# Performance work log

Measured on AMD Instinct MI355X. Metric: run time of the kernel, lower is better.

## Reference

```python
import jax, jax.numpy as jnp
import numpy as np

IN_CHANNELS = 3
WINDOW_SIZE = 11
SIGMA = 1.5
PAD = WINDOW_SIZE // 2


def _create_window():
    # NOTE: faithful to the original repo, the exponent is POSITIVE (a known
    # bug in AntixK/PyTorch-VAE); we replicate the exact math.
    x = np.arange(WINDOW_SIZE, dtype=np.float64)
    k = np.exp((x - WINDOW_SIZE // 2) ** 2 / (2.0 * SIGMA ** 2))
    k = (k / k.sum()).astype(np.float32)
    w2d = np.outer(k, k)  # [K, K]
    # depthwise kernel, OIHW with groups=C -> [C, 1, K, K]
    return jnp.asarray(np.broadcast_to(w2d, (IN_CHANNELS, 1, WINDOW_SIZE, WINDOW_SIZE)).copy())


def _dwconv(x, w):
    return jax.lax.conv_general_dilated(
        x, w, window_strides=(1, 1), padding=[(PAD, PAD), (PAD, PAD)],
        feature_group_count=IN_CHANNELS,
        dimension_numbers=('NCHW', 'OIHW', 'NCHW'))


def _avg_pool2(x):
    B, C, H, W = x.shape
    return x.reshape(B, C, H // 2, 2, W // 2, 2).mean(axis=(3, 5))


def _ssim(img1, img2, window):
    mu1 = _dwconv(img1, window)
    mu2 = _dwconv(img2, window)
    mu1_sq = mu1 * mu1
    mu2_sq = mu2 * mu2
    mu1_mu2 = mu1 * mu2
    sigma1_sq = _dwconv(img1 * img1, window) - mu1_sq
    sigma2_sq = _dwconv(img2 * img2, window) - mu2_sq
    sigma12 = _dwconv(img1 * img2, window) - mu1_mu2
    C1 = 0.01 ** 2
    C2 = 0.03 ** 2
    v1 = 2.0 * sigma12 + C2
    v2 = sigma1_sq + sigma2_sq + C2
    cs = jnp.mean(v1 / v2)
    ssim_map = (2.0 * mu1_mu2 + C1) * v1 / ((mu1_sq + mu2_sq + C1) * v2)
    return jnp.mean(ssim_map), cs  # size_average=True


def setup_inputs() -> dict:
    key = jax.random.key(0)
    k1, k2 = jax.random.split(key)
    shape = (32, 3, 512, 512)
    img1 = jax.random.uniform(k1, shape, dtype=jnp.float32)
    img2 = jax.random.uniform(k2, shape, dtype=jnp.float32)
    return {"img1": img1, "img2": img2}


def reference(img1, img2):
    weights = jnp.asarray([0.0448, 0.2856, 0.3001, 0.2363, 0.1333], dtype=jnp.float32)
    window = _create_window()
    mssim, mcs = [], []
    for _ in range(5):
        sim, cs = _ssim(img1, img2, window)
        mssim.append(sim)
        mcs.append(cs)
        img1 = _avg_pool2(img1)
        img2 = _avg_pool2(img2)
    mssim = jnp.stack(mssim)
    mcs = jnp.stack(mcs)
    pow1 = mcs ** weights
    pow2 = mssim ** weights
    output = jnp.prod(pow1[:-1] * pow2[-1])
    return 1.0 - output
```

## Files before the change

kernel.cpp:

```cpp
#include <hip/hip_runtime.h>
#include <cmath>

typedef short bf16x8 __attribute__((ext_vector_type(8)));
typedef float f32x4 __attribute__((ext_vector_type(4)));

struct Coeffs { float k[11]; };

__device__ __forceinline__ ushort f2bf(float f) {
    unsigned u = __float_as_uint(f);
    u += 0x7fff + ((u >> 16) & 1);
    return (ushort)(u >> 16);
}

__device__ __forceinline__ unsigned pk2(float lo, float hi) {
    unsigned d;
    asm("v_cvt_pk_bf16_f32 %0, %1, %2" : "=v"(d) : "v"(lo), "v"(hi));
    return d;
}

__device__ __forceinline__ float frcp(float x) { return __builtin_amdgcn_rcpf(x); }

__device__ __forceinline__ float4 ld4s(const float* __restrict__ p, int r, int c, int H, int W) {
    float4 v = make_float4(0.f, 0.f, 0.f, 0.f);
    if (r >= 0 && r < H) {
        const float* row = p + (size_t)r * W;
        if (c >= 0 && c + 3 < W) {
            v = *reinterpret_cast<const float4*>(row + c);
        } else {
            if (c + 0 >= 0 && c + 0 < W) v.x = row[c + 0];
            if (c + 1 >= 0 && c + 1 < W) v.y = row[c + 1];
            if (c + 2 >= 0 && c + 2 < W) v.z = row[c + 2];
            if (c + 3 >= 0 && c + 3 < W) v.w = row[c + 3];
        }
    }
    return v;
}

union FragU { ushort us[8]; bf16x8 v; uint4 q; };
union RdU   { uint4 q; bf16x8 v; };

__global__ __launch_bounds__(64)
void init_frag_kernel(uint4* __restrict__ tab, Coeffs cf) {
    const int lane = threadIdx.x;
    const int lj   = lane & 15;
    const int part = lane >> 4;
    FragU bHf, aVf;
    #pragma unroll
    for (int i = 0; i < 8; ++i) {
        const int kk = part * 8 + i;
        const int tH = kk - lj - 3;
        const int tV = kk - lj;
        float vH = 0.f, vV = 0.f;
        #pragma unroll
        for (int tt = 0; tt < 11; ++tt) {
            vH = (tH == tt) ? cf.k[tt] : vH;
            vV = (tV == tt) ? cf.k[tt] : vV;
        }
        bHf.us[i] = f2bf(vH);
        aVf.us[i] = f2bf(vV);
    }
    tab[lane]      = bHf.q;
    tab[64 + lane] = aVf.q;
}

__device__ __forceinline__ void stage_load(const float* __restrict__ p1,
                                           const float* __restrict__ p2,
                                           int H, int W, int gr, int gc0,
                                           float (&a)[12], float (&b)[12]) {
    if (gr >= 0 && gr < H && gc0 >= 0 && gc0 + 12 <= W) {
        const size_t idx = (size_t)gr * W + gc0;
        #pragma unroll
        for (int g = 0; g < 3; ++g) {
            float4 va = *reinterpret_cast<const float4*>(p1 + idx + 4 * g);
            float4 vb = *reinterpret_cast<const float4*>(p2 + idx + 4 * g);
            a[4*g+0]=va.x; a[4*g+1]=va.y; a[4*g+2]=va.z; a[4*g+3]=va.w;
            b[4*g+0]=vb.x; b[4*g+1]=vb.y; b[4*g+2]=vb.z; b[4*g+3]=vb.w;
        }
    } else {
        #pragma unroll
        for (int g = 0; g < 3; ++g) {
            float4 va = ld4s(p1, gr, gc0 + 4 * g, H, W);
            float4 vb = ld4s(p2, gr, gc0 + 4 * g, H, W);
            a[4*g+0]=va.x; a[4*g+1]=va.y; a[4*g+2]=va.z; a[4*g+3]=va.w;
            b[4*g+0]=vb.x; b[4*g+1]=vb.y; b[4*g+2]=vb.z; b[4*g+3]=vb.w;
        }
    }
}

__device__ __forceinline__ void stage_write(const float (&a)[12], const float (&b)[12],
                                            char* q0, char* q1, char* q2) {
    unsigned pks[2][6];
    #pragma unroll
    for (int e = 0; e < 6; ++e) {
        pks[0][e] = pk2(a[2*e], a[2*e+1]);
        pks[1][e] = pk2(b[2*e], b[2*e+1]);
    }
    #pragma unroll
    for (int s = 0; s < 2; ++s) {
        *(uint2*)(q0 + s * 6144) = make_uint2(pks[s][0], pks[s][1]);
        *(uint2*)(q1 + s * 6144) = make_uint2(pks[s][2], pks[s][3]);
        *(uint2*)(q2 + s * 6144) = make_uint2(pks[s][4], pks[s][5]);
    }
}

__device__ __forceinline__ void h_phase(const char* a0p, const char* a1p, char* st,
                                        const bf16x8 bH, const f32x4 zf) {
    #pragma unroll
    for (int cg = 0; cg < 2; ++cg) {
        const char* ap = cg ? a1p : a0p;
        uint4 da = *(const uint4*)(ap);
        uint4 db = *(const uint4*)(ap + 6144);
        unsigned wa[4] = {da.x, da.y, da.z, da.w};
        unsigned wb[4] = {db.x, db.y, db.z, db.w};
        uint4 qaa, qbb, qab;
        unsigned* paa = &qaa.x; unsigned* pbb = &qbb.x; unsigned* pab = &qab.x;
        #pragma unroll
        for (int e = 0; e < 4; ++e) {
            const float alo = __uint_as_float(wa[e] << 16);
            const float ahi = __uint_as_float(wa[e] & 0xffff0000u);
            const float blo = __uint_as_float(wb[e] << 16);
            const float bhi = __uint_as_float(wb[e] & 0xffff0000u);
            paa[e] = pk2(alo * alo, ahi * ahi);
            pbb[e] = pk2(blo * blo, bhi * bhi);
            pab[e] = pk2(alo * blo, ahi * bhi);
        }
        RdU f0, f1, f2, f3, f4;
        f0.q = da; f1.q = db; f2.q = qaa; f3.q = qbb; f4.q = qab;
        f32x4 d0 = __builtin_amdgcn_mfma_f32_16x16x32_bf16(f0.v, bH, zf, 0, 0, 0);
        f32x4 d1 = __builtin_amdgcn_mfma_f32_16x16x32_bf16(f1.v, bH, zf, 0, 0, 0);
        f32x4 d2 = __builtin_amdgcn_mfma_f32_16x16x32_bf16(f2.v, bH, zf, 0, 0, 0);
        f32x4 d3 = __builtin_amdgcn_mfma_f32_16x16x32_bf16(f3.v, bH, zf, 0, 0, 0);
        f32x4 d4 = __builtin_amdgcn_mfma_f32_16x16x32_bf16(f4.v, bH, zf, 0, 0, 0);
        char* sc = st + cg * 2048;
        *(uint2*)(sc)          = make_uint2(pk2(d0[0], d0[1]), pk2(d0[2], d0[3]));
        *(uint2*)(sc + 4096)   = make_uint2(pk2(d1[0], d1[1]), pk2(d1[2], d1[3]));
        *(uint2*)(sc + 8192)   = make_uint2(pk2(d2[0], d2[1]), pk2(d2[2], d2[3]));
        *(uint2*)(sc + 12288)  = make_uint2(pk2(d3[0], d3[1]), pk2(d3[2], d3[3]));
        *(uint2*)(sc + 16384)  = make_uint2(pk2(d4[0], d4[1]), pk2(d4[2], d4[3]));
    }
}

__device__ __forceinline__ void v_phase(const char* hb, const bf16x8 aV, const f32x4 zf,
                                        float& ssim_acc, float& cs_acc) {
    f32x4 acc[5];
    #pragma unroll
    for (int s = 0; s < 5; ++s) {
        RdU br;
        br.q = *(const uint4*)(hb + s * 4096);
        acc[s] = __builtin_amdgcn_mfma_f32_16x16x32_bf16(aV, br.v, zf, 0, 0, 0);
    }
    const float C1 = 1e-4f, C2 = 9e-4f;
    #pragma unroll
    for (int r = 0; r < 4; ++r) {
        const float mu1 = acc[0][r], mu2 = acc[1][r];
        const float m11 = acc[2][r], m22 = acc[3][r], m12 = acc[4][r];
        const float mu1s = mu1 * mu1, mu2s = mu2 * mu2, mu12 = mu1 * mu2;
        const float v1 = 2.f * (m12 - mu12) + C2;
        const float v2 = (m11 - mu1s) + (m22 - mu2s) + C2;
        const float r2 = frcp(v2);
        const float rd = frcp(mu1s + mu2s + C1);
        cs_acc   += v1 * r2;
        ssim_acc += (2.f * mu12 + C1) * v1 * r2 * rd;
    }
}

__device__ __forceinline__ void pool_load8(const float* __restrict__ p1,
                                           const float* __restrict__ p2,
                                           size_t idx, int W, float4 (&P)[8]) {
    P[0] = *reinterpret_cast<const float4*>(p1 + idx);
    P[1] = *reinterpret_cast<const float4*>(p1 + idx + 4);
    P[2] = *reinterpret_cast<const float4*>(p1 + idx + W);
    P[3] = *reinterpret_cast<const float4*>(p1 + idx + W + 4);
    P[4] = *reinterpret_cast<const float4*>(p2 + idx);
    P[5] = *reinterpret_cast<const float4*>(p2 + idx + 4);
    P[6] = *reinterpret_cast<const float4*>(p2 + idx + W);
    P[7] = *reinterpret_cast<const float4*>(p2 + idx + W + 4);
}

__device__ __forceinline__ void pool_store8(const float4 (&P)[8],
                                            float* __restrict__ o1, float* __restrict__ o2,
                                            int bc, int H, int W, int r0, int c0t,
                                            int i, int h) {
    float4 oa, ob;
    oa.x = 0.25f*(P[0].x+P[0].y+P[2].x+P[2].y); oa.y = 0.25f*(P[0].z+P[0].w+P[2].z+P[2].w);
    oa.z = 0.25f*(P[1].x+P[1].y+P[3].x+P[3].y); oa.w = 0.25f*(P[1].z+P[1].w+P[3].z+P[3].w);
    ob.x = 0.25f*(P[4].x+P[4].y+P[6].x+P[6].y); ob.y = 0.25f*(P[4].z+P[4].w+P[6].z+P[6].w);
    ob.z = 0.25f*(P[5].x+P[5].y+P[7].x+P[7].y); ob.w = 0.25f*(P[5].z+P[5].w+P[7].z+P[7].w);
    const int W2 = W >> 1;
    const size_t base = (size_t)bc * (size_t)(H >> 1) * W2
                      + (size_t)(r0/2 + i) * W2 + (c0t/2 + 4*h);
    *reinterpret_cast<float4*>(o1 + base) = oa;
    *reinterpret_cast<float4*>(o2 + base) = ob;
}

__global__ __launch_bounds__(256)
void ssim_level0_mfma(const float* __restrict__ i1, const float* __restrict__ i2,
                      float* __restrict__ o1, float* __restrict__ o2,
                      int H, int W,
                      double* __restrict__ accum,
                      const uint4* __restrict__ frag_tab)
{
    __shared__ __align__(16) ushort A_lds[2][48][64];
    __shared__ __align__(16) ushort H_T [5][32][64];
    __shared__ double red[2][4];

    const int tid  = threadIdx.x;
    const int lane = tid & 63;
    const int lj   = lane & 15;
    const int part = lane >> 4;
    const int swz  = (lane & 7) << 4;
    const int wv   = __builtin_amdgcn_readfirstlane(tid) >> 6;

    const int bc = blockIdx.z;
    const int r0 = blockIdx.y * 32;
    const int c0 = blockIdx.x * 64;
    const float* p1 = i1 + (size_t)bc * H * W;
    const float* p2 = i2 + (size_t)bc * H * W;

    RdU bHu, aVu;
    bHu.q = frag_tab[lane];
    aVu.q = frag_tab[64 + lane];
    const bf16x8 bH = bHu.v;
    const bf16x8 aV = aVu.v;
    const f32x4 zf = {0.f, 0.f, 0.f, 0.f};

    float ssim_acc = 0.f, cs_acc = 0.f;

    float aB[12], bB[12];
    char *q0 = nullptr, *q1 = nullptr, *q2 = nullptr;
    if (tid < 192) {
        const int row_rel = tid >> 2;
        const int colg    = tid & 3;
        const int gr  = r0 - 5 + row_rel;
        const int gcA = c0 - 8 + 12 * colg;
        float aA[12], bA[12];
        stage_load(p1, p2, H, W, gr, gcA,      aA, bA);
        stage_load(p1, p2, H, W, gr, gcA + 32, aB, bB);
        const int cb   = 24 * colg;
        const int swzr = (row_rel & 7) << 4;
        char* base0 = (char*)&A_lds[0][0][0] + row_rel * 128;
        q0 = base0 + ((cb)      ^ swzr);
        q1 = base0 + ((cb + 8)  ^ swzr);
        q2 = base0 + ((cb + 16) ^ swzr);
        stage_write(aA, bA, q0, q1, q2);
    } else if (o1 != nullptr) {
        const int p = tid - 192;
        const int i = p & 15;
        const int h = p >> 4;
        const size_t idxA = (size_t)(r0 + 2 * i) * W + (c0 + 8 * h);
        float4 PA[8], PB[8];
        pool_load8(p1, p2, idxA,      W, PA);
        pool_load8(p1, p2, idxA + 32, W, PB);
        pool_store8(PA, o1, o2, bc, H, W, r0, c0,      i, h);
        pool_store8(PB, o1, o2, bc, H, W, r0, c0 + 32, i, h);
    }
    __syncthreads();

    const char* Ab  = (const char*)&A_lds[0][0][0] + wv * 2048 + lj * 128;
    const char* a0p = Ab + ((part * 16)      ^ swz);
    const char* a1p = Ab + ((32 + part * 16) ^ swz);
    char* st = (char*)&H_T[0][0][0] + lj * 128 + ((wv * 32 + part * 8) ^ swz);
    const int rg2 = wv >> 1, cg2 = wv & 1;
    const char* hb = (const char*)&H_T[0][0][0] + cg2 * 2048 + lj * 128
                   + ((rg2 * 32 + part * 16) ^ swz);

    if (wv < 3) h_phase(a0p, a1p, st, bH, zf);
    __syncthreads();

    if (tid < 192) stage_write(aB, bB, q0, q1, q2);
    v_phase(hb, aV, zf, ssim_acc, cs_acc);
    __syncthreads();

    if (wv < 3) h_phase(a0p, a1p, st, bH, zf);
    __syncthreads();

    v_phase(hb, aV, zf, ssim_acc, cs_acc);

    #pragma unroll
    for (int off = 32; off > 0; off >>= 1) {
        ssim_acc += __shfl_down(ssim_acc, off);
        cs_acc   += __shfl_down(cs_acc, off);
    }
    if (lane == 0) { red[0][wv] = (double)ssim_acc; red[1][wv] = (double)cs_acc; }
    __syncthreads();
    if (tid == 0) {
        double s = red[0][0] + red[0][1] + red[0][2] + red[0][3];
        double c = red[1][0] + red[1][1] + red[1][2] + red[1][3];
        int slot = (blockIdx.x + blockIdx.y * 3 + blockIdx.z * 7) & 63;
        atomicAdd(&accum[slot], s);
        atomicAdd(&accum[64 + slot], c);
    }
}

__global__ __launch_bounds__(256)
void ssim_level1_mfma(const float* __restrict__ i1, const float* __restrict__ i2,
                      float* __restrict__ o1, float* __restrict__ o2,
                      int H, int W,
                      double* __restrict__ accum,
                      const uint4* __restrict__ frag_tab)
{
    __shared__ __align__(16) ushort H_T[5][32][64];
    __shared__ double red[2][4];

    const int tid  = threadIdx.x;
    const int lane = tid & 63;
    const int lj   = lane & 15;
    const int part = lane >> 4;
    const int swz  = (lane & 7) << 4;
    const int wv   = __builtin_amdgcn_readfirstlane(tid) >> 6;

    const int bc = blockIdx.z;
    const int r0 = blockIdx.y * 32;
    const int c0 = blockIdx.x * 32;
    const float* p1 = i1 + (size_t)bc * H * W;
    const float* p2 = i2 + (size_t)bc * H * W;

    RdU bHu, aVu;
    bHu.q = frag_tab[lane];
    aVu.q = frag_tab[64 + lane];
    const bf16x8 bH = bHu.v;
    const bf16x8 aV = aVu.v;

    const f32x4 zf = {0.f, 0.f, 0.f, 0.f};

    if (wv < 3) {
        const int gr = r0 - 5 + wv * 16 + lj;
        char* st = (char*)&H_T[0][0][0] + lj * 128 + ((wv * 32 + part * 8) ^ swz);
        #pragma unroll
        for (int cg = 0; cg < 2; ++cg) {
            const int gc = c0 - 8 + cg * 16 + part * 8;
            float a8[8], b8[8];
            if (gr >= 0 && gr < H && gc >= 0 && gc + 8 <= W) {
                const size_t idx = (size_t)gr * W + gc;
                float4 va0 = *reinterpret_cast<const float4*>(p1 + idx);
                float4 va1 = *reinterpret_cast<const float4*>(p1 + idx + 4);
                float4 vb0 = *reinterpret_cast<const float4*>(p2 + idx);
                float4 vb1 = *reinterpret_cast<const float4*>(p2 + idx + 4);
                a8[0]=va0.x; a8[1]=va0.y; a8[2]=va0.z; a8[3]=va0.w;
                a8[4]=va1.x; a8[5]=va1.y; a8[6]=va1.z; a8[7]=va1.w;
                b8[0]=vb0.x; b8[1]=vb0.y; b8[2]=vb0.z; b8[3]=vb0.w;
                b8[4]=vb1.x; b8[5]=vb1.y; b8[6]=vb1.z; b8[7]=vb1.w;
            } else {
                float4 va0 = ld4s(p1, gr, gc, H, W);
                float4 va1 = ld4s(p1, gr, gc + 4, H, W);
                float4 vb0 = ld4s(p2, gr, gc, H, W);
                float4 vb1 = ld4s(p2, gr, gc + 4, H, W);
                a8[0]=va0.x; a8[1]=va0.y; a8[2]=va0.z; a8[3]=va0.w;
                a8[4]=va1.x; a8[5]=va1.y; a8[6]=va1.z; a8[7]=va1.w;
                b8[0]=vb0.x; b8[1]=vb0.y; b8[2]=vb0.z; b8[3]=vb0.w;
                b8[4]=vb1.x; b8[5]=vb1.y; b8[6]=vb1.z; b8[7]=vb1.w;
            }

            unsigned pkf[5][4];
            #pragma unroll
            for (int e = 0; e < 4; ++e) {
                const float a0 = a8[2*e], a1 = a8[2*e+1];
                const float b0 = b8[2*e], b1 = b8[2*e+1];
                pkf[0][e] = pk2(a0, a1);
                pkf[1][e] = pk2(b0, b1);
                pkf[2][e] = pk2(a0*a0, a1*a1);
                pkf[3][e] = pk2(b0*b0, b1*b1);
                pkf[4][e] = pk2(a0*b0, a1*b1);
            }
            #pragma unroll
            for (int s = 0; s < 5; ++s) {
                RdU fr;
                fr.q.x = pkf[s][0]; fr.q.y = pkf[s][1];
                fr.q.z = pkf[s][2]; fr.q.w = pkf[s][3];
                f32x4 d = __builtin_amdgcn_mfma_f32_16x16x32_bf16(fr.v, bH, zf, 0, 0, 0);
                *(uint2*)(st + cg * 2048 + s * 4096)
                    = make_uint2(pk2(d[0], d[1]), pk2(d[2], d[3]));
            }
        }
    } else if (o1 != nullptr) {
        const int p = tid - 192;
        const int i = p & 15;
        const int h = p >> 4;
        const size_t idx = (size_t)(r0 + 2 * i) * W + (c0 + 8 * h);
        const float* pa = p1 + idx;
        const float* pb = p2 + idx;
        float4 a00 = *reinterpret_cast<const float4*>(pa);
        float4 a01 = *reinterpret_cast<const float4*>(pa + 4);
        float4 a10 = *reinterpret_cast<const float4*>(pa + W);
        float4 a11 = *reinterpret_cast<const float4*>(pa + W + 4);
        float4 b00 = *reinterpret_cast<const float4*>(pb);
        float4 b01 = *reinterpret_cast<const float4*>(pb + 4);
        float4 b10 = *reinterpret_cast<const float4*>(pb + W);
        float4 b11 = *reinterpret_cast<const float4*>(pb + W + 4);
        float4 oa, ob;
        oa.x = 0.25f*(a00.x+a00.y+a10.x+a10.y); oa.y = 0.25f*(a00.z+a00.w+a10.z+a10.w);
        oa.z = 0.25f*(a01.x+a01.y+a11.x+a11.y); oa.w = 0.25f*(a01.z+a01.w+a11.z+a11.w);
        ob.x = 0.25f*(b00.x+b00.y+b10.x+b10.y); ob.y = 0.25f*(b00.z+b00.w+b10.z+b10.w);
        ob.z = 0.25f*(b01.x+b01.y+b11.x+b11.y); ob.w = 0.25f*(b01.z+b01.w+b11.z+b11.w);
        const int W2 = W >> 1;
        const size_t base = (size_t)bc * (size_t)(H >> 1) * W2
                          + (size_t)(r0/2 + i) * W2 + (c0/2 + 4*h);
        *reinterpret_cast<float4*>(o1 + base) = oa;
        *reinterpret_cast<float4*>(o2 + base) = ob;
    }
    __syncthreads();

    const int rg2 = wv >> 1;
    const int cg2 = wv & 1;
    const char* hb = (const char*)&H_T[0][0][0] + cg2 * 2048 + lj * 128
                   + ((rg2 * 32 + part * 16) ^ swz);
    f32x4 acc[5];
    #pragma unroll
    for (int s = 0; s < 5; ++s) {
        RdU br;
        br.q = *(const uint4*)(hb + s * 4096);
        acc[s] = __builtin_amdgcn_mfma_f32_16x16x32_bf16(aV, br.v, zf, 0, 0, 0);
    }

    const float C1 = 1e-4f, C2 = 9e-4f;
    float ssim_acc = 0.f, cs_acc = 0.f;
    #pragma unroll
    for (int r = 0; r < 4; ++r) {
        const float mu1 = acc[0][r], mu2 = acc[1][r];
        const float m11 = acc[2][r], m22 = acc[3][r], m12 = acc[4][r];
        const float mu1s = mu1 * mu1, mu2s = mu2 * mu2, mu12 = mu1 * mu2;
        const float v1 = 2.f * (m12 - mu12) + C2;
        const float v2 = (m11 - mu1s) + (m22 - mu2s) + C2;
        const float r2 = frcp(v2);
        const float rd = frcp(mu1s + mu2s + C1);
        cs_acc   += v1 * r2;
        ssim_acc += (2.f * mu12 + C1) * v1 * r2 * rd;
    }

    #pragma unroll
    for (int off = 32; off > 0; off >>= 1) {
        ssim_acc += __shfl_down(ssim_acc, off);
        cs_acc   += __shfl_down(cs_acc, off);
    }
    if (lane == 0) { red[0][wv] = (double)ssim_acc; red[1][wv] = (double)cs_acc; }
    __syncthreads();
    if (tid == 0) {
        double s = red[0][0] + red[0][1] + red[0][2] + red[0][3];
        double c = red[1][0] + red[1][1] + red[1][2] + red[1][3];
        int slot = (blockIdx.x + blockIdx.y * 3 + blockIdx.z * 7) & 63;
        atomicAdd(&accum[slot], s);
        atomicAdd(&accum[64 + slot], c);
    }
}

#define SPF 33
#define HRF 42

__global__ __launch_bounds__(256)
void ssim_level_f32(const float* __restrict__ i1, const float* __restrict__ i2,
                    float* __restrict__ o1, float* __restrict__ o2,
                    int H, int W,
                    double* __restrict__ accum, Coeffs cf)
{
    __shared__ __align__(16) float varr[5][HRF][SPF];
    __shared__ __align__(16) float phl[2][16][16];
    __shared__ double red[2][4];

    const int tid = threadIdx.x;
    const int bc  = blockIdx.z;
    const int r0 = blockIdx.y * 32;
    const int c0 = blockIdx.x * 32;
    const float* p1 = i1 + (size_t)bc * H * W;
    const float* p2 = i2 + (size_t)bc * H * W;

    const int row_rel = tid >> 2;
    const int j  = tid & 3;
    const int cl = 8 * j;
    float hpA[4], hpB[4];
    bool pool_thread = false;

    if (tid < HRF * 4) {
        const int gr  = r0 + row_rel - 5;
        const int gcb = c0 + cl - 8;

        float a[24], b[24];
        if (gr >= 0 && gr < H && gcb >= 0 && gcb + 24 <= W) {
            const size_t idx = (size_t)gr * W + gcb;
            const float* pa = p1 + idx;
            const float* pb = p2 + idx;
            #pragma unroll
            for (int g = 0; g < 6; ++g) {
                float4 va = *reinterpret_cast<const float4*>(pa + 4 * g);
                float4 vb = *reinterpret_cast<const float4*>(pb + 4 * g);
                a[4*g+0]=va.x; a[4*g+1]=va.y; a[4*g+2]=va.z; a[4*g+3]=va.w;
                b[4*g+0]=vb.x; b[4*g+1]=vb.y; b[4*g+2]=vb.z; b[4*g+3]=vb.w;
            }
        } else {
            #pragma unroll
            for (int g = 0; g < 6; ++g) {
                float4 va = ld4s(p1, gr, gcb + 4 * g, H, W);
                float4 vb = ld4s(p2, gr, gcb + 4 * g, H, W);
                a[4*g+0]=va.x; a[4*g+1]=va.y; a[4*g+2]=va.z; a[4*g+3]=va.w;
                b[4*g+0]=vb.x; b[4*g+1]=vb.y; b[4*g+2]=vb.z; b[4*g+3]=vb.w;
            }
        }

        float acc[5][8] = {};
        #pragma unroll
        for (int i = 0; i < 24; ++i) {
            float av = a[i], bv = b[i];
            float pa2 = av * av, pb2 = bv * bv, pab = av * bv;
            #pragma unroll
            for (int jo = 0; jo < 8; ++jo) {
                const int t = i - 3 - jo;
                if (t >= 0 && t <= 10) {
                    const float kk = cf.k[t];
                    acc[0][jo] += kk * av;  acc[1][jo] += kk * bv;
                    acc[2][jo] += kk * pa2; acc[3][jo] += kk * pb2;
                    acc[4][jo] += kk * pab;
                }
            }
        }
        #pragma unroll
        for (int s = 0; s < 5; ++s) {
            *reinterpret_cast<float4*>(&varr[s][row_rel][cl]) =
                make_float4(acc[s][0], acc[s][1], acc[s][2], acc[s][3]);
            *reinterpret_cast<float4*>(&varr[s][row_rel][cl + 4]) =
                make_float4(acc[s][4], acc[s][5], acc[s][6], acc[s][7]);
        }

        if (o1 != nullptr && row_rel >= 5 && row_rel <= 36) {
            #pragma unroll
            for (int p = 0; p < 4; ++p) {
                hpA[p] = a[8 + 2*p] + a[9 + 2*p];
                hpB[p] = b[8 + 2*p] + b[9 + 2*p];
            }
            if (row_rel & 1) {
                const int i = (row_rel - 5) >> 1;
                *reinterpret_cast<float4*>(&phl[0][i][4*j]) = make_float4(hpA[0],hpA[1],hpA[2],hpA[3]);
                *reinterpret_cast<float4*>(&phl[1][i][4*j]) = make_float4(hpB[0],hpB[1],hpB[2],hpB[3]);
            } else if (row_rel >= 6) {
                pool_thread = true;
            }
        }
    }
    __syncthreads();

    if (pool_thread) {
        const int i = (row_rel - 6) >> 1;
        const int W2 = W >> 1;
        float4 qa = *reinterpret_cast<const float4*>(&phl[0][i][4*j]);
        float4 qb = *reinterpret_cast<const float4*>(&phl[1][i][4*j]);
        qa.x = 0.25f*(qa.x + hpA[0]); qa.y = 0.25f*(qa.y + hpA[1]);
        qa.z = 0.25f*(qa.z + hpA[2]); qa.w = 0.25f*(qa.w + hpA[3]);
        qb.x = 0.25f*(qb.x + hpB[0]); qb.y = 0.25f*(qb.y + hpB[1]);
        qb.z = 0.25f*(qb.z + hpB[2]); qb.w = 0.25f*(qb.w + hpB[3]);
        const size_t base = (size_t)bc * (size_t)(H >> 1) * W2
                          + (size_t)(r0/2 + i) * W2 + (c0/2 + 4*j);
        *reinterpret_cast<float4*>(o1 + base) = qa;
        *reinterpret_cast<float4*>(o2 + base) = qb;
    }

    const int col = tid & 31;
    const int rg  = tid >> 5;

    float acc[5][4] = {};
    #pragma unroll
    for (int t = 0; t < 14; ++t) {
        const int m = rg * 4 + t;
        #pragma unroll
        for (int s = 0; s < 5; ++s) {
            const float val = varr[s][m][col];
            #pragma unroll
            for (int i = 0; i < 4; ++i) {
                const int tap = t - i;
                if (tap >= 0 && tap <= 10) acc[s][i] += cf.k[tap] * val;
            }
        }
    }

    const float C1 = 1e-4f, C2 = 9e-4f;
    float ssim_acc = 0.f, cs_acc = 0.f;
    #pragma unroll
    for (int i = 0; i < 4; ++i) {
        const float mu1 = acc[0][i], mu2 = acc[1][i];
        const float m11 = acc[2][i], m22 = acc[3][i], m12 = acc[4][i];
        const float mu1s = mu1 * mu1, mu2s = mu2 * mu2, mu12 = mu1 * mu2;
        const float v1 = 2.f * (m12 - mu12) + C2;
        const float v2 = (m11 - mu1s) + (m22 - mu2s) + C2;
        const float r2 = frcp(v2);
        const float rd = frcp(mu1s + mu2s + C1);
        cs_acc   += v1 * r2;
        ssim_acc += (2.f * mu12 + C1) * v1 * r2 * rd;
    }

    #pragma unroll
    for (int off = 32; off > 0; off >>= 1) {
        ssim_acc += __shfl_down(ssim_acc, off);
        cs_acc   += __shfl_down(cs_acc, off);
    }
    const int wave = tid >> 6, lane = tid & 63;
    if (lane == 0) { red[0][wave] = (double)ssim_acc; red[1][wave] = (double)cs_acc; }
    __syncthreads();
    if (tid == 0) {
        double s = red[0][0] + red[0][1] + red[0][2] + red[0][3];
        double c = red[1][0] + red[1][1] + red[1][2] + red[1][3];
        int slot = (blockIdx.x + blockIdx.y * 3 + blockIdx.z * 7) & 63;
        atomicAdd(&accum[slot], s);
        atomicAdd(&accum[64 + slot], c);
    }
}

__global__ __launch_bounds__(64)
void finalize_kernel(const double* __restrict__ accum,
                     float* __restrict__ out, int BC)
{
    __shared__ double sums[5][2];
    int tid = threadIdx.x;
    for (int lvl = 0; lvl < 5; ++lvl) {
        for (int m = 0; m < 2; ++m) {
            double v = accum[(lvl * 2 + m) * 64 + tid];
            for (int off = 32; off > 0; off >>= 1) v += __shfl_down(v, off);
            if (tid == 0) sums[lvl][m] = v;
        }
    }
    __syncthreads();
    if (tid == 0) {
        const double w[5] = {0.0448, 0.2856, 0.3001, 0.2363, 0.1333};
        double prod = 1.0;
        for (int lvl = 0; lvl < 5; ++lvl) {
            int hw = (512 >> lvl);
            double cnt = (double)BC * (double)hw * (double)hw;
            double mssim = sums[lvl][0] / cnt;
            double mcs   = sums[lvl][1] / cnt;
            if (lvl < 4) {
                prod *= pow(mcs, w[lvl]);
            } else {
                double p2 = pow(mssim, w[4]);
                prod *= p2 * p2 * p2 * p2;
            }
        }
        out[0] = (float)(1.0 - prod);
    }
}

extern "C" void kernel_launch(void* const* d_in, const int* in_sizes, int n_in,
                              void* d_out, int out_size, void* d_ws, size_t ws_size,
                              hipStream_t stream) {
    const float* img1 = (const float*)d_in[0];
    const float* img2 = (const float*)d_in[1];
    float* out = (float*)d_out;
    char* ws = (char*)d_ws;

    const int BC = in_sizes[0] / (512 * 512);

    double* accum = (double*)ws;
    uint4*  ftab  = (uint4*)(ws + 6144);
    size_t off = 8192;
    float* lvl1[5] = {nullptr, nullptr, nullptr, nullptr, nullptr};
    float* lvl2[5] = {nullptr, nullptr, nullptr, nullptr, nullptr};
    for (int l = 1; l < 5; ++l) {
        size_t hw = (size_t)(512 >> l) * (512 >> l);
        lvl1[l] = (float*)(ws + off); off += (size_t)BC * hw * sizeof(float);
        lvl2[l] = (float*)(ws + off); off += (size_t)BC * hw * sizeof(float);
    }

    hipMemsetAsync(accum, 0, 5 * 2 * 64 * sizeof(double), stream);

    Coeffs cf;
    {
        double kd[11], sum = 0.0;
        for (int i = 0; i < 11; ++i) { kd[i] = exp(((double)((i-5)*(i-5))) / 4.5); sum += kd[i]; }
        for (int i = 0; i < 11; ++i) cf.k[i] = (float)(kd[i] / sum);
    }

    init_frag_kernel<<<1, 64, 0, stream>>>(ftab, cf);

    const float* cur1 = img1;
    const float* cur2 = img2;
    for (int lvl = 0; lvl < 5; ++lvl) {
        int H = 512 >> lvl, W = H;
        float* n1 = (lvl < 4) ? lvl1[lvl + 1] : nullptr;
        float* n2 = (lvl < 4) ? lvl2[lvl + 1] : nullptr;
        if (lvl == 0) {
            dim3 grid(W / 64, H / 32, BC);
            ssim_level0_mfma<<<grid, 256, 0, stream>>>(cur1, cur2, n1, n2, H, W,
                                                       accum + lvl * 128, ftab);
        } else if (lvl == 1) {
            dim3 grid(W / 32, H / 32, BC);
            ssim_level1_mfma<<<grid, 256, 0, stream>>>(cur1, cur2, n1, n2, H, W,
                                                       accum + lvl * 128, ftab);
        } else {
            dim3 grid(W / 32, H / 32, BC);
            ssim_level_f32<<<grid, 256, 0, stream>>>(cur1, cur2, n1, n2, H, W,
                                                     accum + lvl * 128, cf);
        }
        cur1 = n1; cur2 = n2;
    }

    finalize_kernel<<<1, 64, 0, stream>>>(accum, out, BC);
}
```

Measured before the change: 160.4 us.

## Widen level-0 SSIM tiles to 128 columns with pipelined stage loads

Each level-0 block now processes four 32-column strips instead of two, so the grid is halved in x. Global loads for the next strip are issued before the current vertical phase, and pooling loads and stores are interleaved across the strips. The aim is to amortize block setup and fragment-table loads and to hide global-load latency behind MFMA work. The cost is more registers held across phases, which may lower occupancy, and fewer blocks in flight.

```diff
diff --git a/kernel.cpp b/kernel.cpp
--- a/kernel.cpp
+++ b/kernel.cpp
@@ -213,7 +213,7 @@
 
     const int bc = blockIdx.z;
     const int r0 = blockIdx.y * 32;
-    const int c0 = blockIdx.x * 64;
+    const int c0 = blockIdx.x * 128;
     const float* p1 = i1 + (size_t)bc * H * W;
     const float* p2 = i2 + (size_t)bc * H * W;
 
@@ -226,35 +226,26 @@
 
     float ssim_acc = 0.f, cs_acc = 0.f;
 
-    float aB[12], bB[12];
+    const bool stager = (tid < 192);
+    const bool pooler = !stager && (o1 != nullptr);
+
+    const int row_rel = tid >> 2;
+    const int colg    = tid & 3;
+    const int grS  = r0 - 5 + row_rel;
+    const int gcA  = c0 - 8 + 12 * colg;
     char *q0 = nullptr, *q1 = nullptr, *q2 = nullptr;
-    if (tid < 192) {
-        const int row_rel = tid >> 2;
-        const int colg    = tid & 3;
-        const int gr  = r0 - 5 + row_rel;
-        const int gcA = c0 - 8 + 12 * colg;
-        float aA[12], bA[12];
-        stage_load(p1, p2, H, W, gr, gcA,      aA, bA);
-        stage_load(p1, p2, H, W, gr, gcA + 32, aB, bB);
+    {
         const int cb   = 24 * colg;
         const int swzr = (row_rel & 7) << 4;
         char* base0 = (char*)&A_lds[0][0][0] + row_rel * 128;
         q0 = base0 + ((cb)      ^ swzr);
         q1 = base0 + ((cb + 8)  ^ swzr);
         q2 = base0 + ((cb + 16) ^ swzr);
-        stage_write(aA, bA, q0, q1, q2);
-    } else if (o1 != nullptr) {
-        const int p = tid - 192;
-        const int i = p & 15;
-        const int h = p >> 4;
-        const size_t idxA = (size_t)(r0 + 2 * i) * W + (c0 + 8 * h);
-        float4 PA[8], PB[8];
-        pool_load8(p1, p2, idxA,      W, PA);
-        pool_load8(p1, p2, idxA + 32, W, PB);
-        pool_store8(PA, o1, o2, bc, H, W, r0, c0,      i, h);
-        pool_store8(PB, o1, o2, bc, H, W, r0, c0 + 32, i, h);
-    }
-    __syncthreads();
+    }
+
+    const int pi = (tid - 192) & 15;
+    const int ph = (tid - 192) >> 4;
+    const size_t pIdxA = (size_t)(r0 + 2 * pi) * W + (c0 + 8 * ph);
 
     const char* Ab  = (const char*)&A_lds[0][0][0] + wv * 2048 + lj * 128;
     const char* a0p = Ab + ((part * 16)      ^ swz);
@@ -264,16 +255,62 @@
     const char* hb = (const char*)&H_T[0][0][0] + cg2 * 2048 + lj * 128
                    + ((rg2 * 32 + part * 16) ^ swz);
 
+    float aX[12], bX[12], aY[12], bY[12];
+    float4 PX[8], PY[8];
+
+    if (stager) {
+        stage_load(p1, p2, H, W, grS, gcA,      aX, bX);
+        stage_load(p1, p2, H, W, grS, gcA + 32, aY, bY);
+        stage_write(aX, bX, q0, q1, q2);
+    } else if (pooler) {
+        pool_load8(p1, p2, pIdxA, W, PX);
+        pool_store8(PX, o1, o2, bc, H, W, r0, c0, pi, ph);
+    }
+    __syncthreads();
+
     if (wv < 3) h_phase(a0p, a1p, st, bH, zf);
     __syncthreads();
 
-    if (tid < 192) stage_write(aB, bB, q0, q1, q2);
+    if (stager) {
+        stage_load(p1, p2, H, W, grS, gcA + 64, aX, bX);
+        stage_write(aY, bY, q0, q1, q2);
+    } else if (pooler) {
+        pool_load8(p1, p2, pIdxA + 32, W, PX);
+    }
     v_phase(hb, aV, zf, ssim_acc, cs_acc);
     __syncthreads();
 
     if (wv < 3) h_phase(a0p, a1p, st, bH, zf);
     __syncthreads();
 
+    if (stager) {
+        stage_load(p1, p2, H, W, grS, gcA + 96, aY, bY);
+        stage_write(aX, bX, q0, q1, q2);
+    } else if (pooler) {
+        pool_store8(PX, o1, o2, bc, H, W, r0, c0 + 32, pi, ph);
+        pool_load8(p1, p2, pIdxA + 64, W, PY);
+    }
+    v_phase(hb, aV, zf, ssim_acc, cs_acc);
+    __syncthreads();
+
+    if (wv < 3) h_phase(a0p, a1p, st, bH, zf);
+    __syncthreads();
+
+    if (stager) {
+        stage_write(aY, bY, q0, q1, q2);
+    } else if (pooler) {
+        pool_store8(PY, o1, o2, bc, H, W, r0, c0 + 64, pi, ph);
+        pool_load8(p1, p2, pIdxA + 96, W, PX);
+    }
+    v_phase(hb, aV, zf, ssim_acc, cs_acc);
+    __syncthreads();
+
+    if (wv < 3) h_phase(a0p, a1p, st, bH, zf);
+    __syncthreads();
+
+    if (pooler) {
+        pool_store8(PX, o1, o2, bc, H, W, r0, c0 + 96, pi, ph);
+    }
     v_phase(hb, aV, zf, ssim_acc, cs_acc);
 
     #pragma unroll
@@ -673,7 +710,7 @@
         float* n1 = (lvl < 4) ? lvl1[lvl + 1] : nullptr;
         float* n2 = (lvl < 4) ? lvl2[lvl + 1] : nullptr;
         if (lvl == 0) {
-            dim3 grid(W / 64, H / 32, BC);
+            dim3 grid(W / 128, H / 32, BC);
             ssim_level0_mfma<<<grid, 256, 0, stream>>>(cur1, cur2, n1, n2, H, W,
                                                        accum + lvl * 128, ftab);
         } else if (lvl == 1) {
```

Measured after the change: 202.6 us. 1.26x slower.
